# Performance work log

Measured on AMD Instinct MI355X. Metric: run time of the kernel, lower is better.

## Reference

```python
import jax, jax.numpy as jnp
import numpy as np
import math

INPUT_SIZE = 20
HIDDEN = 1500
OUTPUT = 20
MLP_HID = math.ceil(5 / 4 * HIDDEN)  # 1875
T = 4096


def setup_inputs() -> dict:
    key = jax.random.key(0)
    ks = jax.random.split(key, 10)
    s_lstm = 1.0 / np.sqrt(HIDDEN)
    s1 = 1.0 / np.sqrt(HIDDEN)
    s2 = 1.0 / np.sqrt(MLP_HID)
    return {
        "input_seq": jax.random.normal(ks[0], (T, INPUT_SIZE), dtype=jnp.float32),
        "W_ih": jax.random.uniform(ks[1], (4 * HIDDEN, INPUT_SIZE), jnp.float32, -s_lstm, s_lstm),
        "W_hh": jax.random.uniform(ks[2], (4 * HIDDEN, HIDDEN), jnp.float32, -s_lstm, s_lstm),
        "b_ih": jax.random.uniform(ks[3], (4 * HIDDEN,), jnp.float32, -s_lstm, s_lstm),
        "b_hh": jax.random.uniform(ks[4], (4 * HIDDEN,), jnp.float32, -s_lstm, s_lstm),
        "W1": jax.random.uniform(ks[5], (MLP_HID, HIDDEN), jnp.float32, -s1, s1),
        "b1": jax.random.uniform(ks[6], (MLP_HID,), jnp.float32, -s1, s1),
        "W2": jax.random.uniform(ks[7], (OUTPUT, MLP_HID), jnp.float32, -s2, s2),
        "b2": jax.random.uniform(ks[8], (OUTPUT,), jnp.float32, -s2, s2),
    }


def reference(input_seq, W_ih, W_hh, b_ih, b_hh, W1, b1, W2, b2):
    H = W_hh.shape[1]
    # Precompute input contribution for all timesteps: (T, 4H)
    x_proj = input_seq @ W_ih.T + (b_ih + b_hh)

    def step(carry, xp):
        h, c = carry
        gates = xp + h @ W_hh.T  # (4H,)
        i, f, g, o = jnp.split(gates, 4)
        i = jax.nn.sigmoid(i)
        f = jax.nn.sigmoid(f)
        g = jnp.tanh(g)
        o = jax.nn.sigmoid(o)
        c_new = f * c + i * g
        h_new = o * jnp.tanh(c_new)
        return (h_new, c_new), None

    h0 = jnp.zeros((H,), dtype=input_seq.dtype)
    c0 = jnp.zeros((H,), dtype=input_seq.dtype)
    (h_last, _), _ = jax.lax.scan(step, (h0, c0), x_proj)
    # Dropout is identity in eval mode. Module returns predictions[-1],
    # which only depends on the last hidden state.
    hid = h_last @ W1.T + b1
    return hid @ W2.T + b2
```

## Files before the change

kernel.cpp:

```cpp
#include <hip/hip_runtime.h>
#include <math.h>

#define TT 4096
#define HH 1500
#define NB 250
#define NT 512

typedef unsigned long long u64;

#define ALD4(p)   __hip_atomic_load((p), __ATOMIC_RELAXED, __HIP_MEMORY_SCOPE_AGENT)
#define AST4(p,v) __hip_atomic_store((p), (v), __ATOMIC_RELAXED, __HIP_MEMORY_SCOPE_AGENT)

__device__ __forceinline__ float fast_sigmoid(float z) {
  return 1.0f / (1.0f + __expf(-z));
}
__device__ __forceinline__ float fast_tanh(float z) {
  float az = fabsf(z);
  float e  = __expf(-2.0f * az);
  float r  = (1.0f - e) / (1.0f + e);
  return copysignf(r, z);
}

__global__
__attribute__((amdgpu_flat_work_group_size(NT, NT), amdgpu_waves_per_eu(2, 2)))
void lstm_fused(
    const float* __restrict__ x,
    const float* __restrict__ Wih,
    const float* __restrict__ Whh,
    const float* __restrict__ bih,
    const float* __restrict__ bhh,
    const float* __restrict__ W1,
    const float* __restrict__ b1,
    const float* __restrict__ W2,
    const float* __restrict__ b2,
    float* __restrict__ out,
    unsigned* __restrict__ ws)
{
  const int tid = threadIdx.x;
  const int bid = blockIdx.x;
  const int wv  = tid >> 6;
  const int ln  = tid & 63;

  unsigned* pub  = ws;
  unsigned* hidp = ws + 4096;

  __shared__ __align__(16) float lds_w[24 * 1536];
  __shared__ __align__(16) float lds_h[1536];
  __shared__ float lds_xp[2][24];
  __shared__ float lds_gs[4][6];
  float* lds_hd = lds_w;

  if (tid < 36) lds_h[1500 + tid] = 0.0f;

  {
    const float4* whh4 = (const float4*)Whh;
    float4* w4 = (float4*)lds_w;
    for (int idx = tid; idx < 24 * 384; idx += NT) {
      const int r = idx / 384, k4 = idx - r * 384;
      const int u = r >> 2, g = r & 3;
      const int grow = g * HH + bid * 6 + u;
      w4[idx] = (k4 < 375) ? whh4[(size_t)grow * 375 + k4]
                           : make_float4(0.f, 0.f, 0.f, 0.f);
    }
  }

  const float4* h4 = (const float4*)lds_h;
  const int uu = (wv < 6) ? wv : 0;
  const float4* wr0 = (const float4*)lds_w + (size_t)(uu * 4 + 0) * 384;
  const float4* wr1 = (const float4*)lds_w + (size_t)(uu * 4 + 1) * 384;
  const float4* wr2 = (const float4*)lds_w + (size_t)(uu * 4 + 2) * 384;
  const float4* wr3 = (const float4*)lds_w + (size_t)(uu * 4 + 3) * 384;

  float4 wx0, wx1, wx2, wx3, wx4;
  float4 xr0, xr1, xr2, xr3, xr4;
  float bias = 0.f;
  if (wv == 6 && ln < 24) {
    const int g = ln / 6, u = ln - g * 6;
    const int row = g * HH + bid * 6 + u;
    const float4* s = (const float4*)(Wih + row * 20);
    wx0 = s[0]; wx1 = s[1]; wx2 = s[2]; wx3 = s[3]; wx4 = s[4];
    bias = bih[row] + bhh[row];
    const float4* xx = (const float4*)x;
    xr0 = xx[0]; xr1 = xx[1]; xr2 = xx[2]; xr3 = xx[3]; xr4 = xx[4];
  }

  float c = 0.f;

  if (tid < 6) AST4(pub + 0 * 1536 + 6 * bid + tid, 1u);

  __syncthreads();

  for (int t = 0; t < TT; ++t) {
    const int s = t & 1;
    const unsigned tag = (unsigned)((t + 1) & 15);

    float4 pw[12];
    if (wv < 6) {
      #pragma unroll
      for (int g = 0; g < 4; ++g) {
        const float4* wr = (g == 0) ? wr0 : (g == 1) ? wr1 : (g == 2) ? wr2 : wr3;
        #pragma unroll
        for (int m = 0; m < 3; ++m) pw[g * 3 + m] = wr[ln + 64 * m];
      }
    } else {
      if (wv == 6 && ln < 24) {
        float sx = bias;
        sx += wx0.x*xr0.x + wx0.y*xr0.y + wx0.z*xr0.z + wx0.w*xr0.w;
        sx += wx1.x*xr1.x + wx1.y*xr1.y + wx1.z*xr1.z + wx1.w*xr1.w;
        sx += wx2.x*xr2.x + wx2.y*xr2.y + wx2.z*xr2.z + wx2.w*xr2.w;
        sx += wx3.x*xr3.x + wx3.y*xr3.y + wx3.z*xr3.z + wx3.w*xr3.w;
        sx += wx4.x*xr4.x + wx4.y*xr4.y + wx4.z*xr4.z + wx4.w*xr4.w;
        lds_xp[s][ln] = sx;
      }
      const int p = tid - 384;
      unsigned* base = pub + s * 1536;
      unsigned vals[12];
      for (;;) {
        unsigned miss = 0u;
        #pragma unroll
        for (int k = 0; k < 12; ++k) {
          const int idx = p + 128 * k;
          vals[k] = ALD4(base + idx);
          if (idx < HH) miss |= (vals[k] & 15u) ^ tag;
        }
        if (!__any(miss != 0u)) break;
        __builtin_amdgcn_s_sleep(1);
      }
      #pragma unroll
      for (int k = 0; k < 12; ++k) {
        const int idx = p + 128 * k;
        if (idx < HH) lds_h[idx] = __uint_as_float(vals[k]);
      }
    }
    __syncthreads();

    if (wv < 6) {
      float4 hv[6];
      #pragma unroll
      for (int m = 0; m < 6; ++m) hv[m] = h4[ln + 64 * m];
      float4 qw[12];
      #pragma unroll
      for (int g = 0; g < 4; ++g) {
        const float4* wr = (g == 0) ? wr0 : (g == 1) ? wr1 : (g == 2) ? wr2 : wr3;
        #pragma unroll
        for (int m = 0; m < 3; ++m) qw[g * 3 + m] = wr[ln + 64 * (m + 3)];
      }
      float a[4];
      #pragma unroll
      for (int g = 0; g < 4; ++g) {
        float sum = 0.f;
        #pragma unroll
        for (int m = 0; m < 3; ++m) {
          const float4 q = pw[g * 3 + m], hvv = hv[m];
          sum = fmaf(q.x, hvv.x, sum); sum = fmaf(q.y, hvv.y, sum);
          sum = fmaf(q.z, hvv.z, sum); sum = fmaf(q.w, hvv.w, sum);
        }
        #pragma unroll
        for (int m = 0; m < 3; ++m) {
          const float4 q = qw[g * 3 + m], hvv = hv[m + 3];
          sum = fmaf(q.x, hvv.x, sum); sum = fmaf(q.y, hvv.y, sum);
          sum = fmaf(q.z, hvv.z, sum); sum = fmaf(q.w, hvv.w, sum);
        }
        a[g] = sum;
      }
      #pragma unroll
      for (int g = 0; g < 4; ++g) {
        a[g] += __shfl_xor(a[g], 16, 64);
        a[g] += __shfl_xor(a[g], 32, 64);
      }
      const int q4 = ln >> 4;
      float v = (q4 == 0) ? a[0] : (q4 == 1) ? a[1] : (q4 == 2) ? a[2] : a[3];
      v += __shfl_xor(v, 1, 64);
      v += __shfl_xor(v, 2, 64);
      v += __shfl_xor(v, 4, 64);
      v += __shfl_xor(v, 8, 64);
      if ((ln & 15) == 0) lds_gs[q4][wv] = v;
    } else if (wv == 6 && ln < 24 && (t + 1) < TT) {
      const float4* xx = (const float4*)(x + 20 * (t + 1));
      xr0 = xx[0]; xr1 = xx[1]; xr2 = xx[2]; xr3 = xx[3]; xr4 = xx[4];
    }
    __syncthreads();

    if (wv == 7 && ln < 6) {
      const int u = ln;
      const float zi = lds_gs[0][u] + lds_xp[s][0 + u];
      const float zf = lds_gs[1][u] + lds_xp[s][6 + u];
      const float zg = lds_gs[2][u] + lds_xp[s][12 + u];
      const float zo = lds_gs[3][u] + lds_xp[s][18 + u];
      const float ig = fast_sigmoid(zi);
      const float fg = fast_sigmoid(zf);
      const float gg = fast_tanh(zg);
      const float og = fast_sigmoid(zo);
      c = fg * c + ig * gg;
      const float hn = og * fast_tanh(c);
      const unsigned bits = (__float_as_uint(hn) & ~15u) | (unsigned)((t + 2) & 15);
      AST4(pub + ((t + 1) & 1) * 1536 + 6 * bid + u, bits);
    }
  }

  if (wv >= 6) {
    const unsigned tagf = (unsigned)((TT + 1) & 15);
    const int p = tid - 384;
    unsigned* base = pub + 0 * 1536;
    unsigned vals[12];
    for (;;) {
      unsigned miss = 0u;
      #pragma unroll
      for (int k = 0; k < 12; ++k) {
        const int idx = p + 128 * k;
        vals[k] = ALD4(base + idx);
        if (idx < HH) miss |= (vals[k] & 15u) ^ tagf;
      }
      if (!__any(miss != 0u)) break;
      __builtin_amdgcn_s_sleep(1);
    }
    #pragma unroll
    for (int k = 0; k < 12; ++k) {
      const int idx = p + 128 * k;
      if (idx < HH) lds_h[idx] = __uint_as_float(vals[k]);
    }
  }
  __syncthreads();

  {
    const int r = bid + 250 * wv;
    if (r < 1875) {
      const float4* wrow = (const float4*)(W1 + (size_t)r * HH);
      float ss = 0.f;
      #pragma unroll
      for (int m = 0; m < 6; ++m) {
        const int idx = ln + 64 * m;
        if (idx < 375) {
          const float4 a = wrow[idx], hvv = h4[idx];
          ss += a.x*hvv.x + a.y*hvv.y + a.z*hvv.z + a.w*hvv.w;
        }
      }
      #pragma unroll
      for (int off = 32; off > 0; off >>= 1) ss += __shfl_xor(ss, off, 64);
      if (ln == 0) {
        const float vv = ss + b1[r];
        AST4(hidp + r, (__float_as_uint(vv) & ~15u) | 5u);
      }
    }
  }
  if (bid != 0) return;

  __syncthreads();
  for (int j = tid; j < 1875; j += NT) {
    unsigned bts;
    for (;;) {
      bts = ALD4(hidp + j);
      if ((bts & 15u) == 5u) break;
      __builtin_amdgcn_s_sleep(1);
    }
    lds_hd[j] = __uint_as_float(bts);
  }
  __syncthreads();

  for (int r = wv; r < 20; r += 8) {
    float ss = 0.f;
    for (int k = ln; k < 1875; k += 64)
      ss = fmaf(W2[(size_t)r * 1875 + k], lds_hd[k], ss);
    #pragma unroll
    for (int off = 32; off > 0; off >>= 1) ss += __shfl_xor(ss, off, 64);
    if (ln == 0) out[r] = ss + b2[r];
  }
}

extern "C" void kernel_launch(void* const* d_in, const int* in_sizes, int n_in,
                              void* d_out, int out_size, void* d_ws, size_t ws_size,
                              hipStream_t stream) {
  const float* x   = (const float*)d_in[0];
  const float* Wih = (const float*)d_in[1];
  const float* Whh = (const float*)d_in[2];
  const float* bih = (const float*)d_in[3];
  const float* bhh = (const float*)d_in[4];
  const float* W1  = (const float*)d_in[5];
  const float* b1  = (const float*)d_in[6];
  const float* W2  = (const float*)d_in[7];
  const float* b2  = (const float*)d_in[8];
  float* out   = (float*)d_out;
  unsigned* ws = (unsigned*)d_ws;

  hipLaunchKernelGGL(lstm_fused, dim3(NB), dim3(NT), 0, stream,
                     x, Wih, Whh, bih, bhh, W1, b1, W2, b2, out, ws);
}
```

Before: 12.70 ms.

## Poll published hidden state directly into compute waves, drop LDS staging and a barrier

The six compute waves now poll the published h vector themselves with inline dwordx4 global loads (sc1), keeping h in registers instead of staging it through LDS. This removes one __syncthreads per timestep and the LDS round trip. Block size drops from 8 to 7 waves. The input projection is now computed in wave 6 and passed by shuffle rather than through LDS, and that wave also does the gate update. The cost is heavier per-wave polling traffic and more register pressure from 24 preloaded weight float4s, and the inline asm relies on sc1 cache semantics being correct for coherence.

After: 15.58 ms. 22.7% more time.

```diff
diff --git a/kernel.cpp b/kernel.cpp
--- a/kernel.cpp
+++ b/kernel.cpp
@@ -4,9 +4,9 @@
 #define TT 4096
 #define HH 1500
 #define NB 250
-#define NT 512
-
-typedef unsigned long long u64;
+#define NT 448
+
+typedef unsigned uv4 __attribute__((ext_vector_type(4)));
 
 #define ALD4(p)   __hip_atomic_load((p), __ATOMIC_RELAXED, __HIP_MEMORY_SCOPE_AGENT)
 #define AST4(p,v) __hip_atomic_store((p), (v), __ATOMIC_RELAXED, __HIP_MEMORY_SCOPE_AGENT)
@@ -46,11 +46,8 @@
 
   __shared__ __align__(16) float lds_w[24 * 1536];
   __shared__ __align__(16) float lds_h[1536];
-  __shared__ float lds_xp[2][24];
   __shared__ float lds_gs[4][6];
   float* lds_hd = lds_w;
-
-  if (tid < 36) lds_h[1500 + tid] = 0.0f;
 
   {
     const float4* whh4 = (const float4*)Whh;
@@ -64,7 +61,6 @@
     }
   }
 
-  const float4* h4 = (const float4*)lds_h;
   const int uu = (wv < 6) ? wv : 0;
   const float4* wr0 = (const float4*)lds_w + (size_t)(uu * 4 + 0) * 384;
   const float4* wr1 = (const float4*)lds_w + (size_t)(uu * 4 + 1) * 384;
@@ -86,7 +82,7 @@
 
   float c = 0.f;
 
-  if (tid < 6) AST4(pub + 0 * 1536 + 6 * bid + tid, 1u);
+  if (tid < 6) AST4(pub + 6 * bid + tid, 1u);
 
   __syncthreads();
 
@@ -94,72 +90,73 @@
     const int s = t & 1;
     const unsigned tag = (unsigned)((t + 1) & 15);
 
-    float4 pw[12];
     if (wv < 6) {
+      float4 qw[24];
       #pragma unroll
       for (int g = 0; g < 4; ++g) {
         const float4* wr = (g == 0) ? wr0 : (g == 1) ? wr1 : (g == 2) ? wr2 : wr3;
         #pragma unroll
-        for (int m = 0; m < 3; ++m) pw[g * 3 + m] = wr[ln + 64 * m];
-      }
-    } else {
-      if (wv == 6 && ln < 24) {
-        float sx = bias;
-        sx += wx0.x*xr0.x + wx0.y*xr0.y + wx0.z*xr0.z + wx0.w*xr0.w;
-        sx += wx1.x*xr1.x + wx1.y*xr1.y + wx1.z*xr1.z + wx1.w*xr1.w;
-        sx += wx2.x*xr2.x + wx2.y*xr2.y + wx2.z*xr2.z + wx2.w*xr2.w;
-        sx += wx3.x*xr3.x + wx3.y*xr3.y + wx3.z*xr3.z + wx3.w*xr3.w;
-        sx += wx4.x*xr4.x + wx4.y*xr4.y + wx4.z*xr4.z + wx4.w*xr4.w;
-        lds_xp[s][ln] = sx;
-      }
-      const int p = tid - 384;
-      unsigned* base = pub + s * 1536;
-      unsigned vals[12];
+        for (int m = 0; m < 6; ++m) qw[g * 6 + m] = wr[ln + 64 * m];
+      }
+      asm volatile("" ::: "memory");
+
+      const unsigned* bp  = pub + (size_t)s * 1536 + 4 * ln;
+      const unsigned* bp2 = bp + 1024;
+      uv4 h0, h1, h2, h3, h4v, h5;
       for (;;) {
-        unsigned miss = 0u;
-        #pragma unroll
-        for (int k = 0; k < 12; ++k) {
-          const int idx = p + 128 * k;
-          vals[k] = ALD4(base + idx);
-          if (idx < HH) miss |= (vals[k] & 15u) ^ tag;
+        asm volatile(
+          "global_load_dwordx4 %0, %6, off sc1\n\t"
+          "global_load_dwordx4 %1, %6, off offset:1024 sc1\n\t"
+          "global_load_dwordx4 %2, %6, off offset:2048 sc1\n\t"
+          "global_load_dwordx4 %3, %6, off offset:3072 sc1\n\t"
+          "global_load_dwordx4 %4, %7, off sc1\n\t"
+          "global_load_dwordx4 %5, %7, off offset:1024 sc1\n\t"
+          "s_waitcnt vmcnt(0)"
+          : "=v"(h0), "=v"(h1), "=v"(h2), "=v"(h3), "=v"(h4v), "=v"(h5)
+          : "v"(bp), "v"(bp2)
+          : "memory");
+        unsigned miss = ((h0.x & 15u) ^ tag) | ((h0.y & 15u) ^ tag) |
+                        ((h0.z & 15u) ^ tag) | ((h0.w & 15u) ^ tag);
+        miss |= ((h1.x & 15u) ^ tag) | ((h1.y & 15u) ^ tag) |
+                ((h1.z & 15u) ^ tag) | ((h1.w & 15u) ^ tag);
+        miss |= ((h2.x & 15u) ^ tag) | ((h2.y & 15u) ^ tag) |
+                ((h2.z & 15u) ^ tag) | ((h2.w & 15u) ^ tag);
+        miss |= ((h3.x & 15u) ^ tag) | ((h3.y & 15u) ^ tag) |
+                ((h3.z & 15u) ^ tag) | ((h3.w & 15u) ^ tag);
+        miss |= ((h4v.x & 15u) ^ tag) | ((h4v.y & 15u) ^ tag) |
+                ((h4v.z & 15u) ^ tag) | ((h4v.w & 15u) ^ tag);
+        if (ln < 55) {
+          miss |= ((h5.x & 15u) ^ tag) | ((h5.y & 15u) ^ tag) |
+                  ((h5.z & 15u) ^ tag) | ((h5.w & 15u) ^ tag);
         }
         if (!__any(miss != 0u)) break;
         __builtin_amdgcn_s_sleep(1);
       }
-      #pragma unroll
-      for (int k = 0; k < 12; ++k) {
-        const int idx = p + 128 * k;
-        if (idx < HH) lds_h[idx] = __uint_as_float(vals[k]);
-      }
-    }
-    __syncthreads();
-
-    if (wv < 6) {
-      float4 hv[6];
-      #pragma unroll
-      for (int m = 0; m < 6; ++m) hv[m] = h4[ln + 64 * m];
-      float4 qw[12];
-      #pragma unroll
-      for (int g = 0; g < 4; ++g) {
-        const float4* wr = (g == 0) ? wr0 : (g == 1) ? wr1 : (g == 2) ? wr2 : wr3;
-        #pragma unroll
-        for (int m = 0; m < 3; ++m) qw[g * 3 + m] = wr[ln + 64 * (m + 3)];
-      }
+      float4 hf[6];
+      hf[0] = make_float4(__uint_as_float(h0.x), __uint_as_float(h0.y),
+                          __uint_as_float(h0.z), __uint_as_float(h0.w));
+      hf[1] = make_float4(__uint_as_float(h1.x), __uint_as_float(h1.y),
+                          __uint_as_float(h1.z), __uint_as_float(h1.w));
+      hf[2] = make_float4(__uint_as_float(h2.x), __uint_as_float(h2.y),
+                          __uint_as_float(h2.z), __uint_as_float(h2.w));
+      hf[3] = make_float4(__uint_as_float(h3.x), __uint_as_float(h3.y),
+                          __uint_as_float(h3.z), __uint_as_float(h3.w));
+      hf[4] = make_float4(__uint_as_float(h4v.x), __uint_as_float(h4v.y),
+                          __uint_as_float(h4v.z), __uint_as_float(h4v.w));
+      hf[5] = (ln < 55)
+            ? make_float4(__uint_as_float(h5.x), __uint_as_float(h5.y),
+                          __uint_as_float(h5.z), __uint_as_float(h5.w))
+            : make_float4(0.f, 0.f, 0.f, 0.f);
+
       float a[4];
       #pragma unroll
       for (int g = 0; g < 4; ++g) {
         float sum = 0.f;
         #pragma unroll
-        for (int m = 0; m < 3; ++m) {
-          const float4 q = pw[g * 3 + m], hvv = hv[m];
-          sum = fmaf(q.x, hvv.x, sum); sum = fmaf(q.y, hvv.y, sum);
-          sum = fmaf(q.z, hvv.z, sum); sum = fmaf(q.w, hvv.w, sum);
-        }
-        #pragma unroll
-        for (int m = 0; m < 3; ++m) {
-          const float4 q = qw[g * 3 + m], hvv = hv[m + 3];
-          sum = fmaf(q.x, hvv.x, sum); sum = fmaf(q.y, hvv.y, sum);
-          sum = fmaf(q.z, hvv.z, sum); sum = fmaf(q.w, hvv.w, sum);
+        for (int m = 0; m < 6; ++m) {
+          const float4 q = qw[g * 6 + m], hv = hf[m];
+          sum = fmaf(q.x, hv.x, sum); sum = fmaf(q.y, hv.y, sum);
+          sum = fmaf(q.z, hv.z, sum); sum = fmaf(q.w, hv.w, sum);
         }
         a[g] = sum;
       }
@@ -175,71 +172,94 @@
       v += __shfl_xor(v, 4, 64);
       v += __shfl_xor(v, 8, 64);
       if ((ln & 15) == 0) lds_gs[q4][wv] = v;
-    } else if (wv == 6 && ln < 24 && (t + 1) < TT) {
-      const float4* xx = (const float4*)(x + 20 * (t + 1));
-      xr0 = xx[0]; xr1 = xx[1]; xr2 = xx[2]; xr3 = xx[3]; xr4 = xx[4];
+    }
+
+    float xi = 0.f, xf = 0.f, xg = 0.f, xo = 0.f;
+    if (wv == 6) {
+      float xpv = 0.f;
+      if (ln < 24) {
+        float sx = bias;
+        sx += wx0.x*xr0.x + wx0.y*xr0.y + wx0.z*xr0.z + wx0.w*xr0.w;
+        sx += wx1.x*xr1.x + wx1.y*xr1.y + wx1.z*xr1.z + wx1.w*xr1.w;
+        sx += wx2.x*xr2.x + wx2.y*xr2.y + wx2.z*xr2.z + wx2.w*xr2.w;
+        sx += wx3.x*xr3.x + wx3.y*xr3.y + wx3.z*xr3.z + wx3.w*xr3.w;
+        sx += wx4.x*xr4.x + wx4.y*xr4.y + wx4.z*xr4.z + wx4.w*xr4.w;
+        xpv = sx;
+      }
+      xi = __shfl(xpv, ln, 64);
+      xf = __shfl(xpv, ln + 6, 64);
+      xg = __shfl(xpv, ln + 12, 64);
+      xo = __shfl(xpv, ln + 18, 64);
     }
     __syncthreads();
 
-    if (wv == 7 && ln < 6) {
-      const int u = ln;
-      const float zi = lds_gs[0][u] + lds_xp[s][0 + u];
-      const float zf = lds_gs[1][u] + lds_xp[s][6 + u];
-      const float zg = lds_gs[2][u] + lds_xp[s][12 + u];
-      const float zo = lds_gs[3][u] + lds_xp[s][18 + u];
-      const float ig = fast_sigmoid(zi);
-      const float fg = fast_sigmoid(zf);
-      const float gg = fast_tanh(zg);
-      const float og = fast_sigmoid(zo);
-      c = fg * c + ig * gg;
-      const float hn = og * fast_tanh(c);
-      const unsigned bits = (__float_as_uint(hn) & ~15u) | (unsigned)((t + 2) & 15);
-      AST4(pub + ((t + 1) & 1) * 1536 + 6 * bid + u, bits);
-    }
-  }
-
-  if (wv >= 6) {
-    const unsigned tagf = (unsigned)((TT + 1) & 15);
-    const int p = tid - 384;
-    unsigned* base = pub + 0 * 1536;
-    unsigned vals[12];
+    if (wv == 6) {
+      if (ln < 6) {
+        const int u = ln;
+        const float zi = lds_gs[0][u] + xi;
+        const float zf = lds_gs[1][u] + xf;
+        const float zg = lds_gs[2][u] + xg;
+        const float zo = lds_gs[3][u] + xo;
+        const float ig = fast_sigmoid(zi);
+        const float fg = fast_sigmoid(zf);
+        const float gg = fast_tanh(zg);
+        const float og = fast_sigmoid(zo);
+        c = fg * c + ig * gg;
+        const float hn = og * fast_tanh(c);
+        const unsigned bits = (__float_as_uint(hn) & ~15u) | (unsigned)((t + 2) & 15);
+        AST4(pub + ((t + 1) & 1) * 1536 + 6 * bid + u, bits);
+      }
+      if (ln < 24 && (t + 1) < TT) {
+        const float4* xx = (const float4*)(x + 20 * (t + 1));
+        xr0 = xx[0]; xr1 = xx[1]; xr2 = xx[2]; xr3 = xx[3]; xr4 = xx[4];
+      }
+    }
+  }
+
+  if (wv < 6) {
+    const int fi = ln + 64 * wv;
+    const unsigned* bp = pub + 4 * fi;
+    uv4 hx;
     for (;;) {
+      asm volatile("global_load_dwordx4 %0, %1, off sc1\n\ts_waitcnt vmcnt(0)"
+                   : "=v"(hx) : "v"(bp) : "memory");
       unsigned miss = 0u;
-      #pragma unroll
-      for (int k = 0; k < 12; ++k) {
-        const int idx = p + 128 * k;
-        vals[k] = ALD4(base + idx);
-        if (idx < HH) miss |= (vals[k] & 15u) ^ tagf;
+      if (fi < 375) {
+        miss = ((hx.x & 15u) ^ 1u) | ((hx.y & 15u) ^ 1u) |
+               ((hx.z & 15u) ^ 1u) | ((hx.w & 15u) ^ 1u);
       }
       if (!__any(miss != 0u)) break;
       __builtin_amdgcn_s_sleep(1);
     }
-    #pragma unroll
-    for (int k = 0; k < 12; ++k) {
-      const int idx = p + 128 * k;
-      if (idx < HH) lds_h[idx] = __uint_as_float(vals[k]);
-    }
+    float4 hfv = (fi < 375)
+               ? make_float4(__uint_as_float(hx.x), __uint_as_float(hx.y),
+                             __uint_as_float(hx.z), __uint_as_float(hx.w))
+               : make_float4(0.f, 0.f, 0.f, 0.f);
+    ((float4*)lds_h)[fi] = hfv;
   }
   __syncthreads();
 
   {
-    const int r = bid + 250 * wv;
-    if (r < 1875) {
-      const float4* wrow = (const float4*)(W1 + (size_t)r * HH);
-      float ss = 0.f;
-      #pragma unroll
-      for (int m = 0; m < 6; ++m) {
-        const int idx = ln + 64 * m;
-        if (idx < 375) {
-          const float4 a = wrow[idx], hvv = h4[idx];
-          ss += a.x*hvv.x + a.y*hvv.y + a.z*hvv.z + a.w*hvv.w;
+    const float4* h4 = (const float4*)lds_h;
+    for (int i = wv; i < 8; i += 7) {
+      const int r = bid + 250 * i;
+      if (r < 1875) {
+        const float4* wrow = (const float4*)(W1 + (size_t)r * HH);
+        float ss = 0.f;
+        #pragma unroll
+        for (int m = 0; m < 6; ++m) {
+          const int idx = ln + 64 * m;
+          if (idx < 375) {
+            const float4 a = wrow[idx], hv = h4[idx];
+            ss += a.x*hv.x + a.y*hv.y + a.z*hv.z + a.w*hv.w;
+          }
         }
-      }
-      #pragma unroll
-      for (int off = 32; off > 0; off >>= 1) ss += __shfl_xor(ss, off, 64);
-      if (ln == 0) {
-        const float vv = ss + b1[r];
-        AST4(hidp + r, (__float_as_uint(vv) & ~15u) | 5u);
+        #pragma unroll
+        for (int off = 32; off > 0; off >>= 1) ss += __shfl_xor(ss, off, 64);
+        if (ln == 0) {
+          const float vv = ss + b1[r];
+          AST4(hidp + r, (__float_as_uint(vv) & ~15u) | 5u);
+        }
       }
     }
   }
@@ -257,7 +277,7 @@
   }
   __syncthreads();
 
-  for (int r = wv; r < 20; r += 8) {
+  for (int r = wv; r < 20; r += 7) {
     float ss = 0.f;
     for (int k = ln; k < 1875; k += 64)
       ss = fmaf(W2[(size_t)r * 1875 + k], lds_hd[k], ss);
```
